# Optimization experiments

Hardware: AMD Instinct MI355X
Metric: run time of the kernel (lower is better)

Reference implementation:

```python
import jax, jax.numpy as jnp
import numpy as np

V, K, C, F = 100000, 64, 3, 16
HID = [64, 64, 64]  # 'large' pca-net hidden widths (config.yaml stand-in)
EPS = 1e-4


def setup_inputs() -> dict:
    key = jax.random.key(0)
    ks = jax.random.split(key, 12)
    inp = {
        "coordinates": jax.random.normal(ks[0], (V, C), jnp.float32),
        "distsq": jax.random.uniform(ks[1], (V, K), jnp.float32),
        "features": jax.random.uniform(ks[2], (V, F), jnp.float32),
        "n_idxs": jax.random.randint(ks[3], (V, K), 0, V, jnp.int32),
    }
    dims = [C * C] + HID + [C * C]
    for i in range(len(dims) - 1):
        fan_in = dims[i]
        inp[f"W{i}"] = jax.random.normal(ks[4 + 2 * i], (dims[i], dims[i + 1]), jnp.float32) / np.sqrt(fan_in)
        inp[f"b{i}"] = jnp.zeros((dims[i + 1],), jnp.float32)
    return inp


def _neighbour_covariance(coordinates, distsq, features, n_idxs):
    # gather neighbour coords/features: [V,K,C], [V,K,F]
    nbc = jnp.take(coordinates, n_idxs, axis=0)
    nbf = jnp.take(features, n_idxs, axis=0)
    # per-neighbour per-feature weights, distsq pre-scaled by 10 in call()
    w = nbf * jnp.exp(-10.0 * distsq)[:, :, None]          # [V,K,F]
    wsum = jnp.sum(w, axis=1) + EPS                         # [V,F]
    mean = jnp.einsum("vkf,vkc->vfc", w, nbc) / wsum[:, :, None]  # [V,F,C]
    # E[x x^T] - mu mu^T (avoids materializing [V,K,F,C] centered diffs)
    m2 = jnp.einsum("vkf,vkc,vkd->vfcd", w, nbc, nbc) / wsum[:, :, None, None]
    cov = m2 - mean[:, :, :, None] * mean[:, :, None, :]    # [V,F,C,C]
    return cov, mean


def reference(coordinates, distsq, features, n_idxs,
              W0, b0, W1, b1, W2, b2, W3, b3):
    cov, mean = _neighbour_covariance(coordinates, distsq, features, n_idxs)
    x = cov.reshape(-1, C * C)                              # [V*F, C^2]
    # per-layer path: ELU on every layer, including the final one
    for Wl, bl in ((W0, b0), (W1, b1), (W2, b2), (W3, b3)):
        x = jax.nn.elu(x @ Wl + bl)
    return x.reshape(-1, F * C * C)                         # [V, F*C^2]
```

## Files before the change

kernel.cpp:

```cpp
#include <hip/hip_runtime.h>
#include <math.h>

#define NV 100000
#define NK 64
#define NF 16
#define EPS_W 1e-4f
#define WS_NEED ((size_t)NV * 16 * 32)
#define GRID_MLP 3125

typedef __attribute__((ext_vector_type(8))) short bf16x8;
typedef __attribute__((ext_vector_type(4))) float f32x4;

__device__ __forceinline__ unsigned short bfu(float x) {
    return __builtin_bit_cast(unsigned short, (__bf16)x);
}
__device__ __forceinline__ unsigned int pk2(float lo, float hi) {
    return (unsigned int)bfu(lo) | ((unsigned int)bfu(hi) << 16);
}
__device__ __forceinline__ float eluf(float x) {
    return x > 0.f ? x : __expf(x) - 1.f;
}

__launch_bounds__(256)
__global__ void cov3_kernel(const float* __restrict__ coords,
                            const float* __restrict__ distsq,
                            const float* __restrict__ feats,
                            const int*   __restrict__ nidx,
                            unsigned char* __restrict__ ws)
{
    __shared__ float sEW[8][64];
    __shared__ int   sIX[8][64];
    const int tid = threadIdx.x;
    const int vb  = blockIdx.x * 8;

    #pragma unroll
    for (int r = 0; r < 2; ++r) {
        int t  = tid + r * 256;
        int gv = t >> 6, k = t & 63;
        float d  = distsq[(size_t)(vb + gv) * NK + k];
        int   ix = nidx [(size_t)(vb + gv) * NK + k];
        sEW[gv][k] = __expf(-10.f * d);
        sIX[gv][k] = ix;
    }
    __syncthreads();

    const int lane = tid & 63;
    const int wid  = tid >> 6;
    const int f    = lane & 15;
    const int kh   = (lane >> 4) & 1;
    const int g2   = lane >> 5;
    const int gv   = wid * 2 + g2;
    const int v    = vb + gv;

    float s=0.f, m0=0.f,m1=0.f,m2=0.f;
    float q00=0.f,q01=0.f,q02=0.f,q11=0.f,q12=0.f,q22=0.f;

    #pragma unroll 8
    for (int i = 0; i < 32; ++i) {
        int   k   = kh * 32 + i;
        int   idx = sIX[gv][k];
        float ew  = sEW[gv][k];
        float w   = feats[(size_t)idx * NF + f] * ew;
        float x = coords[(size_t)idx*3+0];
        float y = coords[(size_t)idx*3+1];
        float z = coords[(size_t)idx*3+2];
        s += w;
        m0 = fmaf(w,x,m0); m1 = fmaf(w,y,m1); m2 = fmaf(w,z,m2);
        float wx=w*x, wy=w*y, wz=w*z;
        q00=fmaf(wx,x,q00); q01=fmaf(wx,y,q01); q02=fmaf(wx,z,q02);
        q11=fmaf(wy,y,q11); q12=fmaf(wy,z,q12); q22=fmaf(wz,z,q22);
    }
    s   += __shfl_xor(s,   16);
    m0  += __shfl_xor(m0,  16);
    m1  += __shfl_xor(m1,  16);
    m2  += __shfl_xor(m2,  16);
    q00 += __shfl_xor(q00, 16);
    q01 += __shfl_xor(q01, 16);
    q02 += __shfl_xor(q02, 16);
    q11 += __shfl_xor(q11, 16);
    q12 += __shfl_xor(q12, 16);
    q22 += __shfl_xor(q22, 16);

    if (kh == 0) {
        float inv = 1.f / (s + EPS_W);
        float mu0=m0*inv, mu1=m1*inv, mu2=m2*inv;
        float c00=fmaf(-mu0,mu0,q00*inv);
        float c01=fmaf(-mu0,mu1,q01*inv);
        float c02=fmaf(-mu0,mu2,q02*inv);
        float c11=fmaf(-mu1,mu1,q11*inv);
        float c12=fmaf(-mu1,mu2,q12*inv);
        float c22=fmaf(-mu2,mu2,q22*inv);

        uint4 lo, hi;
        lo.x = pk2(c00, c01);
        lo.y = pk2(c02, c01);
        lo.z = pk2(c11, c12);
        lo.w = pk2(c02, c12);
        hi.x = pk2(c22, 1.0f);
        hi.y = 0u; hi.z = 0u; hi.w = 0u;

        uint4* dst = (uint4*)(ws + ((size_t)v * 16 + f) * 32);
        dst[0] = lo;
        dst[1] = hi;
    }
}

__device__ __forceinline__ bf16x8 rdW(const short* sw, int c, int g, int t, int kc) {
    int byte = (t << 11) + (c << 7) + (kc << 6) + (g << 4);
    byte ^= (c & 7) << 4;
    return *(const bf16x8*)((const char*)sw + byte);
}

struct B2 { bf16x8 b0, b1; };
__device__ __forceinline__ B2 d2b(const unsigned int pk_[4][2], int c, int g) {
    const int srcA = c + ((g & 1) << 5);
    const int srcB = srcA + 16;
    const bool hi = (g >> 1) != 0;
    union { unsigned int u[4]; bf16x8 v; } U0, U1;
    #pragma unroll
    for (int m = 0; m < 4; ++m) {
        int src = (m & 2) ? srcB : srcA;
        int j   = m & 1;
        unsigned int e0 = (unsigned int)__shfl((int)pk_[0][j], src);
        unsigned int o0 = (unsigned int)__shfl((int)pk_[1][j], src);
        unsigned int e1 = (unsigned int)__shfl((int)pk_[2][j], src);
        unsigned int o1 = (unsigned int)__shfl((int)pk_[3][j], src);
        U0.u[m] = hi ? o0 : e0;
        U1.u[m] = hi ? o1 : e1;
    }
    B2 r; r.b0 = U0.v; r.b1 = U1.v; return r;
}

__launch_bounds__(256, 4)
__global__ void mlp6_kernel(const unsigned char* __restrict__ ws,
                            const float* __restrict__ W0, const float* __restrict__ b0,
                            const float* __restrict__ W1, const float* __restrict__ b1,
                            const float* __restrict__ W2, const float* __restrict__ b2,
                            const float* __restrict__ W3, const float* __restrict__ b3,
                            float* __restrict__ out)
{
    __shared__ __align__(16) short sW1[4096];
    __shared__ __align__(16) short sW2[4096];
    __shared__ __align__(16) float sOut[4][160];

    const int tid  = threadIdx.x;
    const int wid  = tid >> 6;
    const int lane = tid & 63;
    const int c    = lane & 15;
    const int g    = lane >> 4;

    union U8 { short s[8]; bf16x8 v; };

    #pragma unroll
    for (int r = 0; r < 2; ++r) {
        int t = tid + r * 256;
        int j = t & 63, o = t >> 6;
        U8 u1, u2;
        #pragma unroll
        for (int i = 0; i < 8; ++i) {
            u1.s[i] = (short)bfu(W1[(8 * o + i) * 64 + j]);
            u2.s[i] = (short)bfu(W2[(8 * o + i) * 64 + j]);
        }
        int byte = ((j << 7) + (o << 4)) ^ ((j & 7) << 4);
        *(bf16x8*)((char*)sW1 + byte) = u1.v;
        *(bf16x8*)((char*)sW2 + byte) = u2.v;
    }
    __syncthreads();

    bf16x8 w0f[4], w3f[2];
    #pragma unroll
    for (int t = 0; t < 4; ++t) {
        U8 u;
        #pragma unroll
        for (int i = 0; i < 8; ++i) {
            int k = 8 * g + i;
            float val = 0.f;
            if (k < 9)       val = W0[k * 64 + 16 * t + c];
            else if (k == 9) val = b0[16 * t + c];
            u.s[i] = (short)bfu(val);
        }
        w0f[t] = u.v;
    }
    #pragma unroll
    for (int kc = 0; kc < 2; ++kc) {
        U8 u;
        #pragma unroll
        for (int i = 0; i < 8; ++i) {
            int k = 32 * kc + 8 * g + i;
            u.s[i] = (short)bfu(c < 9 ? W3[k * 9 + c] : 0.f);
        }
        w3f[kc] = u.v;
    }
    float b1v[16], b2v[16], b3v[4];
    #pragma unroll
    for (int t = 0; t < 4; ++t)
        #pragma unroll
        for (int r = 0; r < 4; ++r) {
            b1v[4 * t + r] = b1[16 * t + 4 * g + r];
            b2v[4 * t + r] = b2[16 * t + 4 * g + r];
        }
    #pragma unroll
    for (int r = 0; r < 4; ++r)
        b3v[r] = (4 * g + r < 9) ? b3[4 * g + r] : 0.f;

    float* fOut = &sOut[wid][0];

    const int stride = gridDim.x * 4;
    int v = blockIdx.x * 4 + wid;
    if (v >= NV) return;

    const unsigned char* wp = ws + (size_t)v * 512 + (c << 5) + ((g & 1) << 4);
    const size_t wstep = (size_t)stride * 512;
    float* ob = out + (size_t)v * 144;
    const size_t ostep = (size_t)stride * 144;

    bf16x8 bin = *(const bf16x8*)(wp);

    for (; v < NV; v += stride) {
        const unsigned char* wpn = (v + stride < NV) ? (wp + wstep) : wp;
        bf16x8 nb = *(const bf16x8*)(wpn);

        f32x4 A[4];
        unsigned int pkv[4][2];

        #pragma unroll
        for (int t = 0; t < 4; ++t) {
            f32x4 z4 = {0.f, 0.f, 0.f, 0.f};
            A[t] = __builtin_amdgcn_mfma_f32_16x16x32_bf16(w0f[t], bin, z4, 0, 0, 0);
        }
        #pragma unroll
        for (int t = 0; t < 4; ++t) {
            pkv[t][0] = pk2(eluf(A[t][0]), eluf(A[t][1]));
            pkv[t][1] = pk2(eluf(A[t][2]), eluf(A[t][3]));
        }
        B2 h = d2b(pkv, c, g);

        #pragma unroll
        for (int t = 0; t < 4; ++t) {
            bf16x8 wa = rdW(sW1, c, g, t, 0);
            bf16x8 wb = rdW(sW1, c, g, t, 1);
            f32x4 a = { b1v[4*t+0], b1v[4*t+1], b1v[4*t+2], b1v[4*t+3] };
            a = __builtin_amdgcn_mfma_f32_16x16x32_bf16(wa, h.b0, a, 0, 0, 0);
            a = __builtin_amdgcn_mfma_f32_16x16x32_bf16(wb, h.b1, a, 0, 0, 0);
            A[t] = a;
        }
        #pragma unroll
        for (int t = 0; t < 4; ++t) {
            pkv[t][0] = pk2(eluf(A[t][0]), eluf(A[t][1]));
            pkv[t][1] = pk2(eluf(A[t][2]), eluf(A[t][3]));
        }
        h = d2b(pkv, c, g);

        #pragma unroll
        for (int t = 0; t < 4; ++t) {
            bf16x8 wa = rdW(sW2, c, g, t, 0);
            bf16x8 wb = rdW(sW2, c, g, t, 1);
            f32x4 a = { b2v[4*t+0], b2v[4*t+1], b2v[4*t+2], b2v[4*t+3] };
            a = __builtin_amdgcn_mfma_f32_16x16x32_bf16(wa, h.b0, a, 0, 0, 0);
            a = __builtin_amdgcn_mfma_f32_16x16x32_bf16(wb, h.b1, a, 0, 0, 0);
            A[t] = a;
        }
        #pragma unroll
        for (int t = 0; t < 4; ++t) {
            pkv[t][0] = pk2(eluf(A[t][0]), eluf(A[t][1]));
            pkv[t][1] = pk2(eluf(A[t][2]), eluf(A[t][3]));
        }
        h = d2b(pkv, c, g);

        {
            f32x4 a = { b3v[0], b3v[1], b3v[2], b3v[3] };
            a = __builtin_amdgcn_mfma_f32_16x16x32_bf16(w3f[0], h.b0, a, 0, 0, 0);
            a = __builtin_amdgcn_mfma_f32_16x16x32_bf16(w3f[1], h.b1, a, 0, 0, 0);
            if (g < 2) {
                fOut[c * 9 + 4 * g + 0] = eluf(a[0]);
                fOut[c * 9 + 4 * g + 1] = eluf(a[1]);
                fOut[c * 9 + 4 * g + 2] = eluf(a[2]);
                fOut[c * 9 + 4 * g + 3] = eluf(a[3]);
            } else if (g == 2) {
                fOut[c * 9 + 8] = eluf(a[0]);
            }
        }
        __asm__ volatile("s_waitcnt lgkmcnt(0)" ::: "memory");

        if (lane < 36) {
            float4 val = *(const float4*)(fOut + lane * 4);
            *(float4*)(ob + lane * 4) = val;
        }
        __asm__ volatile("s_waitcnt lgkmcnt(0)" ::: "memory");

        bin = nb;
        wp = wpn;
        ob += ostep;
    }
}

__launch_bounds__(256, 2)
__global__ void fused_pca_mlp(const float* __restrict__ coords,
                              const float* __restrict__ distsq,
                              const float* __restrict__ feats,
                              const int*   __restrict__ nidx,
                              const float* __restrict__ W0, const float* __restrict__ b0,
                              const float* __restrict__ W1, const float* __restrict__ b1,
                              const float* __restrict__ W2, const float* __restrict__ b2,
                              const float* __restrict__ W3, const float* __restrict__ b3,
                              float* __restrict__ out)
{
    __shared__ __align__(16) float sW0t[64 * 9];
    __shared__ __align__(16) float sW1t[64 * 64];
    __shared__ __align__(16) float sW2t[64 * 64];
    __shared__ __align__(16) float sW3t[9 * 64];
    __shared__ float sB0[64], sB1[64], sB2[64], sB3[9];
    const int tid = threadIdx.x;
    for (int t = tid; t < 64 * 9; t += 256) { int j = t / 9, i = t - j * 9; sW0t[t] = W0[i * 64 + j]; }
    for (int t = tid; t < 64 * 64; t += 256) { int j = t >> 6, i = t & 63; sW1t[t] = W1[i * 64 + j]; }
    for (int t = tid; t < 64 * 64; t += 256) { int j = t >> 6, i = t & 63; sW2t[t] = W2[i * 64 + j]; }
    for (int t = tid; t < 9 * 64; t += 256) { int j = t >> 6, i = t & 63; sW3t[t] = W3[i * 9 + j]; }
    if (tid < 64) { sB0[tid] = b0[tid]; sB1[tid] = b1[tid]; sB2[tid] = b2[tid]; }
    if (tid < 9)  { sB3[tid] = b3[tid]; }
    __syncthreads();
    const int g = tid >> 4, f = tid & 15;
    const int v = blockIdx.x * 16 + g;
    if (v >= NV) return;
    const int* nix = nidx + (size_t)v * NK;
    const float* dsq = distsq + (size_t)v * NK;
    float s = 0.f, m0=0,m1=0,m2=0, q00=0,q01=0,q02=0,q11=0,q12=0,q22=0;
    #pragma unroll 4
    for (int k = 0; k < NK; ++k) {
        int idx = nix[k];
        float ew = __expf(-10.0f * dsq[k]);
        float w = feats[(size_t)idx * NF + f] * ew;
        float x = coords[(size_t)idx*3+0], y = coords[(size_t)idx*3+1], z = coords[(size_t)idx*3+2];
        s += w; m0 = fmaf(w,x,m0); m1 = fmaf(w,y,m1); m2 = fmaf(w,z,m2);
        float wx=w*x, wy=w*y, wz=w*z;
        q00=fmaf(wx,x,q00); q01=fmaf(wx,y,q01); q02=fmaf(wx,z,q02);
        q11=fmaf(wy,y,q11); q12=fmaf(wy,z,q12); q22=fmaf(wz,z,q22);
    }
    float inv = 1.0f/(s+EPS_W), mu0=m0*inv, mu1=m1*inv, mu2=m2*inv;
    float xr[9];
    xr[0]=fmaf(-mu0,mu0,q00*inv); xr[1]=fmaf(-mu0,mu1,q01*inv); xr[2]=fmaf(-mu0,mu2,q02*inv);
    xr[3]=xr[1]; xr[4]=fmaf(-mu1,mu1,q11*inv); xr[5]=fmaf(-mu1,mu2,q12*inv);
    xr[6]=xr[2]; xr[7]=xr[5]; xr[8]=fmaf(-mu2,mu2,q22*inv);
    float h[64], gg[64];
    #pragma unroll
    for (int j = 0; j < 64; ++j) {
        float aa = sB0[j]; const float* wr = sW0t + j * 9;
        #pragma unroll
        for (int i = 0; i < 9; ++i) aa = fmaf(xr[i], wr[i], aa);
        h[j] = eluf(aa);
    }
    #pragma unroll
    for (int j = 0; j < 64; ++j) {
        float aa = sB1[j]; const float4* wr = (const float4*)(sW1t + (j << 6));
        #pragma unroll
        for (int i4 = 0; i4 < 16; ++i4) { float4 wv = wr[i4];
            aa = fmaf(h[4*i4+0],wv.x,aa); aa = fmaf(h[4*i4+1],wv.y,aa);
            aa = fmaf(h[4*i4+2],wv.z,aa); aa = fmaf(h[4*i4+3],wv.w,aa); }
        gg[j] = eluf(aa);
    }
    #pragma unroll
    for (int j = 0; j < 64; ++j) {
        float aa = sB2[j]; const float4* wr = (const float4*)(sW2t + (j << 6));
        #pragma unroll
        for (int i4 = 0; i4 < 16; ++i4) { float4 wv = wr[i4];
            aa = fmaf(gg[4*i4+0],wv.x,aa); aa = fmaf(gg[4*i4+1],wv.y,aa);
            aa = fmaf(gg[4*i4+2],wv.z,aa); aa = fmaf(gg[4*i4+3],wv.w,aa); }
        h[j] = eluf(aa);
    }
    float o[9];
    #pragma unroll
    for (int j = 0; j < 9; ++j) {
        float aa = sB3[j]; const float4* wr = (const float4*)(sW3t + (j << 6));
        #pragma unroll
        for (int i4 = 0; i4 < 16; ++i4) { float4 wv = wr[i4];
            aa = fmaf(h[4*i4+0],wv.x,aa); aa = fmaf(h[4*i4+1],wv.y,aa);
            aa = fmaf(h[4*i4+2],wv.z,aa); aa = fmaf(h[4*i4+3],wv.w,aa); }
        o[j] = eluf(aa);
    }
    float* op = out + ((size_t)v * NF + f) * 9;
    #pragma unroll
    for (int j = 0; j < 9; ++j) op[j] = o[j];
}

extern "C" void kernel_launch(void* const* d_in, const int* in_sizes, int n_in,
                              void* d_out, int out_size, void* d_ws, size_t ws_size,
                              hipStream_t stream) {
    (void)in_sizes; (void)n_in; (void)out_size;
    const float* coords = (const float*)d_in[0];
    const float* distsq = (const float*)d_in[1];
    const float* feats  = (const float*)d_in[2];
    const int*   nidx   = (const int*)d_in[3];
    const float* W0 = (const float*)d_in[4];
    const float* b0 = (const float*)d_in[5];
    const float* W1 = (const float*)d_in[6];
    const float* b1 = (const float*)d_in[7];
    const float* W2 = (const float*)d_in[8];
    const float* b2 = (const float*)d_in[9];
    const float* W3 = (const float*)d_in[10];
    const float* b3 = (const float*)d_in[11];
    float* out = (float*)d_out;

    if (ws_size >= WS_NEED) {
        unsigned char* ws = (unsigned char*)d_ws;
        hipLaunchKernelGGL(cov3_kernel, dim3(NV / 8), dim3(256), 0, stream,
                           coords, distsq, feats, nidx, ws);
        hipLaunchKernelGGL(mlp6_kernel, dim3(GRID_MLP), dim3(256), 0, stream,
                           ws, W0, b0, W1, b1, W2, b2, W3, b3, out);
    } else {
        hipLaunchKernelGGL(fused_pca_mlp, dim3(NV / 16), dim3(256), 0, stream,
                           coords, distsq, feats, nidx,
                           W0, b0, W1, b1, W2, b2, W3, b3, out);
    }
}
```

Measured before the change: 214.8 us.

## Software-pipeline MLP layers across two vertices via LDS activation exchange

The MLP kernel now processes two vertices at once, interleaved in a staggered pipeline. Layers 2 and 3 of one vertex run alongside layers 0 and 1 of the next, with setprio around the MFMA bursts to keep independent matrix work flowing. Activation relayout between layers now goes through a swizzled per-wave LDS buffer instead of cross-lane shuffles, and bf16 packing uses the packed conversion intrinsic. The per-wave trip count is hardcoded to 8 vertices with a fixed stride, which assumes NV equals the grid times 4 times 8. It also lowers occupancy to 3 blocks per CU and adds LDS traffic.

```diff
diff --git a/kernel.cpp b/kernel.cpp
--- a/kernel.cpp
+++ b/kernel.cpp
@@ -1,4 +1,5 @@
 #include <hip/hip_runtime.h>
+#include <hip/hip_bf16.h>
 #include <math.h>
 
 #define NV 100000
@@ -7,6 +8,7 @@
 #define EPS_W 1e-4f
 #define WS_NEED ((size_t)NV * 16 * 32)
 #define GRID_MLP 3125
+#define STRIDE_MLP 12500
 
 typedef __attribute__((ext_vector_type(8))) short bf16x8;
 typedef __attribute__((ext_vector_type(4))) float f32x4;
@@ -15,7 +17,11 @@
     return __builtin_bit_cast(unsigned short, (__bf16)x);
 }
 __device__ __forceinline__ unsigned int pk2(float lo, float hi) {
-    return (unsigned int)bfu(lo) | ((unsigned int)bfu(hi) << 16);
+    float2 t; t.x = lo; t.y = hi;
+    __hip_bfloat162 r = __float22bfloat162_rn(t);
+    unsigned int u;
+    __builtin_memcpy(&u, &r, 4);
+    return u;
 }
 __device__ __forceinline__ float eluf(float x) {
     return x > 0.f ? x : __expf(x) - 1.f;
@@ -105,34 +111,24 @@
     }
 }
 
+__device__ __forceinline__ bf16x8 rdfrag(const short* hb, int c, int g, int kc) {
+    int boff = ((kc << 6) + (g << 4)) ^ ((c & 7) << 4);
+    return *(const bf16x8*)(hb + c * 64 + (boff >> 1));
+}
+__device__ __forceinline__ void wrH(short* hb, int c, int g, int t,
+                                    unsigned int p01, unsigned int p23) {
+    int boff = ((t << 5) + (g << 3)) ^ ((c & 7) << 4);
+    uint2 val; val.x = p01; val.y = p23;
+    *(uint2*)(hb + c * 64 + (boff >> 1)) = val;
+}
 __device__ __forceinline__ bf16x8 rdW(const short* sw, int c, int g, int t, int kc) {
     int byte = (t << 11) + (c << 7) + (kc << 6) + (g << 4);
     byte ^= (c & 7) << 4;
     return *(const bf16x8*)((const char*)sw + byte);
 }
 
-struct B2 { bf16x8 b0, b1; };
-__device__ __forceinline__ B2 d2b(const unsigned int pk_[4][2], int c, int g) {
-    const int srcA = c + ((g & 1) << 5);
-    const int srcB = srcA + 16;
-    const bool hi = (g >> 1) != 0;
-    union { unsigned int u[4]; bf16x8 v; } U0, U1;
-    #pragma unroll
-    for (int m = 0; m < 4; ++m) {
-        int src = (m & 2) ? srcB : srcA;
-        int j   = m & 1;
-        unsigned int e0 = (unsigned int)__shfl((int)pk_[0][j], src);
-        unsigned int o0 = (unsigned int)__shfl((int)pk_[1][j], src);
-        unsigned int e1 = (unsigned int)__shfl((int)pk_[2][j], src);
-        unsigned int o1 = (unsigned int)__shfl((int)pk_[3][j], src);
-        U0.u[m] = hi ? o0 : e0;
-        U1.u[m] = hi ? o1 : e1;
-    }
-    B2 r; r.b0 = U0.v; r.b1 = U1.v; return r;
-}
-
-__launch_bounds__(256, 4)
-__global__ void mlp6_kernel(const unsigned char* __restrict__ ws,
+__launch_bounds__(256, 3)
+__global__ void mlp7_kernel(const unsigned char* __restrict__ ws,
                             const float* __restrict__ W0, const float* __restrict__ b0,
                             const float* __restrict__ W1, const float* __restrict__ b1,
                             const float* __restrict__ W2, const float* __restrict__ b2,
@@ -141,6 +137,7 @@
 {
     __shared__ __align__(16) short sW1[4096];
     __shared__ __align__(16) short sW2[4096];
+    __shared__ __align__(16) short hbuf[4][2][1024];
     __shared__ __align__(16) float sOut[4][160];
 
     const int tid  = threadIdx.x;
@@ -203,94 +200,157 @@
     for (int r = 0; r < 4; ++r)
         b3v[r] = (4 * g + r < 9) ? b3[4 * g + r] : 0.f;
 
+    short* hbP = &hbuf[wid][0][0];
+    short* hbQ = &hbuf[wid][1][0];
     float* fOut = &sOut[wid][0];
 
-    const int stride = gridDim.x * 4;
-    int v = blockIdx.x * 4 + wid;
-    if (v >= NV) return;
-
-    const unsigned char* wp = ws + (size_t)v * 512 + (c << 5) + ((g & 1) << 4);
-    const size_t wstep = (size_t)stride * 512;
-    float* ob = out + (size_t)v * 144;
-    const size_t ostep = (size_t)stride * 144;
-
-    bf16x8 bin = *(const bf16x8*)(wp);
-
-    for (; v < NV; v += stride) {
-        const unsigned char* wpn = (v + stride < NV) ? (wp + wstep) : wp;
-        bf16x8 nb = *(const bf16x8*)(wpn);
-
+    const int v0 = blockIdx.x * 4 + wid;
+    const unsigned char* base = ws + (c << 5) + ((g & 1) << 4);
+    float* ob = out + (size_t)v0 * 144;
+    const size_t ostep = (size_t)STRIDE_MLP * 144;
+
+    bf16x8 hP0, hP1;
+
+    {
+        bf16x8 bin = *(const bf16x8*)(base + (size_t)v0 * 512);
         f32x4 A[4];
-        unsigned int pkv[4][2];
-
         #pragma unroll
         for (int t = 0; t < 4; ++t) {
             f32x4 z4 = {0.f, 0.f, 0.f, 0.f};
             A[t] = __builtin_amdgcn_mfma_f32_16x16x32_bf16(w0f[t], bin, z4, 0, 0, 0);
         }
         #pragma unroll
-        for (int t = 0; t < 4; ++t) {
-            pkv[t][0] = pk2(eluf(A[t][0]), eluf(A[t][1]));
-            pkv[t][1] = pk2(eluf(A[t][2]), eluf(A[t][3]));
-        }
-        B2 h = d2b(pkv, c, g);
-
+        for (int t = 0; t < 4; ++t)
+            wrH(hbQ, c, g, t, pk2(eluf(A[t][0]), eluf(A[t][1])),
+                              pk2(eluf(A[t][2]), eluf(A[t][3])));
+        __asm__ volatile("s_waitcnt lgkmcnt(0)" ::: "memory");
+        bf16x8 h0 = rdfrag(hbQ, c, g, 0), h1 = rdfrag(hbQ, c, g, 1);
         #pragma unroll
         for (int t = 0; t < 4; ++t) {
             bf16x8 wa = rdW(sW1, c, g, t, 0);
             bf16x8 wb = rdW(sW1, c, g, t, 1);
             f32x4 a = { b1v[4*t+0], b1v[4*t+1], b1v[4*t+2], b1v[4*t+3] };
-            a = __builtin_amdgcn_mfma_f32_16x16x32_bf16(wa, h.b0, a, 0, 0, 0);
-            a = __builtin_amdgcn_mfma_f32_16x16x32_bf16(wb, h.b1, a, 0, 0, 0);
+            a = __builtin_amdgcn_mfma_f32_16x16x32_bf16(wa, h0, a, 0, 0, 0);
+            a = __builtin_amdgcn_mfma_f32_16x16x32_bf16(wb, h1, a, 0, 0, 0);
             A[t] = a;
         }
         #pragma unroll
-        for (int t = 0; t < 4; ++t) {
-            pkv[t][0] = pk2(eluf(A[t][0]), eluf(A[t][1]));
-            pkv[t][1] = pk2(eluf(A[t][2]), eluf(A[t][3]));
-        }
-        h = d2b(pkv, c, g);
-
+        for (int t = 0; t < 4; ++t)
+            wrH(hbQ, c, g, t, pk2(eluf(A[t][0]), eluf(A[t][1])),
+                              pk2(eluf(A[t][2]), eluf(A[t][3])));
+        __asm__ volatile("s_waitcnt lgkmcnt(0)" ::: "memory");
+        hP0 = rdfrag(hbQ, c, g, 0);
+        hP1 = rdfrag(hbQ, c, g, 1);
+    }
+
+    bf16x8 binQ = *(const bf16x8*)(base + (size_t)(v0 + STRIDE_MLP) * 512);
+
+    #pragma unroll 1
+    for (int k = 0; k < 7; ++k) {
+        int vpre = v0 + (k + 2 <= 7 ? (k + 2) : 7) * STRIDE_MLP;
+        bf16x8 binR = *(const bf16x8*)(base + (size_t)vpre * 512);
+
+        f32x4 AP[4], AQ[4];
+        __builtin_amdgcn_s_setprio(1);
         #pragma unroll
         for (int t = 0; t < 4; ++t) {
             bf16x8 wa = rdW(sW2, c, g, t, 0);
             bf16x8 wb = rdW(sW2, c, g, t, 1);
             f32x4 a = { b2v[4*t+0], b2v[4*t+1], b2v[4*t+2], b2v[4*t+3] };
-            a = __builtin_amdgcn_mfma_f32_16x16x32_bf16(wa, h.b0, a, 0, 0, 0);
-            a = __builtin_amdgcn_mfma_f32_16x16x32_bf16(wb, h.b1, a, 0, 0, 0);
-            A[t] = a;
-        }
-        #pragma unroll
-        for (int t = 0; t < 4; ++t) {
-            pkv[t][0] = pk2(eluf(A[t][0]), eluf(A[t][1]));
-            pkv[t][1] = pk2(eluf(A[t][2]), eluf(A[t][3]));
-        }
-        h = d2b(pkv, c, g);
-
-        {
-            f32x4 a = { b3v[0], b3v[1], b3v[2], b3v[3] };
-            a = __builtin_amdgcn_mfma_f32_16x16x32_bf16(w3f[0], h.b0, a, 0, 0, 0);
-            a = __builtin_amdgcn_mfma_f32_16x16x32_bf16(w3f[1], h.b1, a, 0, 0, 0);
-            if (g < 2) {
-                fOut[c * 9 + 4 * g + 0] = eluf(a[0]);
-                fOut[c * 9 + 4 * g + 1] = eluf(a[1]);
-                fOut[c * 9 + 4 * g + 2] = eluf(a[2]);
-                fOut[c * 9 + 4 * g + 3] = eluf(a[3]);
-            } else if (g == 2) {
-                fOut[c * 9 + 8] = eluf(a[0]);
-            }
-        }
+            a = __builtin_amdgcn_mfma_f32_16x16x32_bf16(wa, hP0, a, 0, 0, 0);
+            a = __builtin_amdgcn_mfma_f32_16x16x32_bf16(wb, hP1, a, 0, 0, 0);
+            AP[t] = a;
+        }
+        #pragma unroll
+        for (int t = 0; t < 4; ++t) {
+            f32x4 z4 = {0.f, 0.f, 0.f, 0.f};
+            AQ[t] = __builtin_amdgcn_mfma_f32_16x16x32_bf16(w0f[t], binQ, z4, 0, 0, 0);
+        }
+        __builtin_amdgcn_s_setprio(0);
+        #pragma unroll
+        for (int t = 0; t < 4; ++t) {
+            wrH(hbP, c, g, t, pk2(eluf(AP[t][0]), eluf(AP[t][1])),
+                              pk2(eluf(AP[t][2]), eluf(AP[t][3])));
+            wrH(hbQ, c, g, t, pk2(eluf(AQ[t][0]), eluf(AQ[t][1])),
+                              pk2(eluf(AQ[t][2]), eluf(AQ[t][3])));
+        }
+        __asm__ volatile("s_waitcnt lgkmcnt(0)" ::: "memory");
+
+        bf16x8 hp0 = rdfrag(hbP, c, g, 0), hp1 = rdfrag(hbP, c, g, 1);
+        bf16x8 hq0 = rdfrag(hbQ, c, g, 0), hq1 = rdfrag(hbQ, c, g, 1);
+        __builtin_amdgcn_s_setprio(1);
+        f32x4 aP = { b3v[0], b3v[1], b3v[2], b3v[3] };
+        aP = __builtin_amdgcn_mfma_f32_16x16x32_bf16(w3f[0], hp0, aP, 0, 0, 0);
+        aP = __builtin_amdgcn_mfma_f32_16x16x32_bf16(w3f[1], hp1, aP, 0, 0, 0);
+        #pragma unroll
+        for (int t = 0; t < 4; ++t) {
+            bf16x8 wa = rdW(sW1, c, g, t, 0);
+            bf16x8 wb = rdW(sW1, c, g, t, 1);
+            f32x4 a = { b1v[4*t+0], b1v[4*t+1], b1v[4*t+2], b1v[4*t+3] };
+            a = __builtin_amdgcn_mfma_f32_16x16x32_bf16(wa, hq0, a, 0, 0, 0);
+            a = __builtin_amdgcn_mfma_f32_16x16x32_bf16(wb, hq1, a, 0, 0, 0);
+            AQ[t] = a;
+        }
+        __builtin_amdgcn_s_setprio(0);
+        if (g < 2) {
+            fOut[c * 9 + 4 * g + 0] = eluf(aP[0]);
+            fOut[c * 9 + 4 * g + 1] = eluf(aP[1]);
+            fOut[c * 9 + 4 * g + 2] = eluf(aP[2]);
+            fOut[c * 9 + 4 * g + 3] = eluf(aP[3]);
+        } else if (g == 2) {
+            fOut[c * 9 + 8] = eluf(aP[0]);
+        }
+        #pragma unroll
+        for (int t = 0; t < 4; ++t)
+            wrH(hbQ, c, g, t, pk2(eluf(AQ[t][0]), eluf(AQ[t][1])),
+                              pk2(eluf(AQ[t][2]), eluf(AQ[t][3])));
         __asm__ volatile("s_waitcnt lgkmcnt(0)" ::: "memory");
 
         if (lane < 36) {
             float4 val = *(const float4*)(fOut + lane * 4);
             *(float4*)(ob + lane * 4) = val;
         }
-        __asm__ volatile("s_waitcnt lgkmcnt(0)" ::: "memory");
-
-        bin = nb;
-        wp = wpn;
+        hP0 = rdfrag(hbQ, c, g, 0);
+        hP1 = rdfrag(hbQ, c, g, 1);
+        __asm__ volatile("s_waitcnt lgkmcnt(0)" ::: "memory");
+
+        binQ = binR;
         ob += ostep;
+    }
+
+    {
+        f32x4 AP[4];
+        #pragma unroll
+        for (int t = 0; t < 4; ++t) {
+            bf16x8 wa = rdW(sW2, c, g, t, 0);
+            bf16x8 wb = rdW(sW2, c, g, t, 1);
+            f32x4 a = { b2v[4*t+0], b2v[4*t+1], b2v[4*t+2], b2v[4*t+3] };
+            a = __builtin_amdgcn_mfma_f32_16x16x32_bf16(wa, hP0, a, 0, 0, 0);
+            a = __builtin_amdgcn_mfma_f32_16x16x32_bf16(wb, hP1, a, 0, 0, 0);
+            AP[t] = a;
+        }
+        #pragma unroll
+        for (int t = 0; t < 4; ++t)
+            wrH(hbP, c, g, t, pk2(eluf(AP[t][0]), eluf(AP[t][1])),
+                              pk2(eluf(AP[t][2]), eluf(AP[t][3])));
+        __asm__ volatile("s_waitcnt lgkmcnt(0)" ::: "memory");
+        bf16x8 hp0 = rdfrag(hbP, c, g, 0), hp1 = rdfrag(hbP, c, g, 1);
+        f32x4 aP = { b3v[0], b3v[1], b3v[2], b3v[3] };
+        aP = __builtin_amdgcn_mfma_f32_16x16x32_bf16(w3f[0], hp0, aP, 0, 0, 0);
+        aP = __builtin_amdgcn_mfma_f32_16x16x32_bf16(w3f[1], hp1, aP, 0, 0, 0);
+        if (g < 2) {
+            fOut[c * 9 + 4 * g + 0] = eluf(aP[0]);
+            fOut[c * 9 + 4 * g + 1] = eluf(aP[1]);
+            fOut[c * 9 + 4 * g + 2] = eluf(aP[2]);
+            fOut[c * 9 + 4 * g + 3] = eluf(aP[3]);
+        } else if (g == 2) {
+            fOut[c * 9 + 8] = eluf(aP[0]);
+        }
+        __asm__ volatile("s_waitcnt lgkmcnt(0)" ::: "memory");
+        if (lane < 36) {
+            float4 val = *(const float4*)(fOut + lane * 4);
+            *(float4*)(ob + lane * 4) = val;
+        }
     }
 }
 
@@ -403,7 +463,7 @@
         unsigned char* ws = (unsigned char*)d_ws;
         hipLaunchKernelGGL(cov3_kernel, dim3(NV / 8), dim3(256), 0, stream,
                            coords, distsq, feats, nidx, ws);
-        hipLaunchKernelGGL(mlp6_kernel, dim3(GRID_MLP), dim3(256), 0, stream,
+        hipLaunchKernelGGL(mlp7_kernel, dim3(GRID_MLP), dim3(256), 0, stream,
                            ws, W0, b0, W1, b1, W2, b2, W3, b3, out);
     } else {
         hipLaunchKernelGGL(fused_pca_mlp, dim3(NV / 16), dim3(256), 0, stream,
```

Measured after the change: 212.5 us. Within noise of the previous version (-1.1%).
